# Kernel tuning notes

Measured on AMD Instinct MI355X. Metric: run time of the kernel, lower is better.

The kernel has to match this reference:

```python
import jax, jax.numpy as jnp
import numpy as np

ALPHA = jnp.full((8,), 0.25, dtype=jnp.float32)  # per-class focal alpha
GAMMA = 2.0
TEMP = 0.07
CIRC_TARGET = 1.0
CIRC_WEIGHT = 0.1
MIN_AGREE = 0.6
W_FOCAL, W_CONTRAST, W_CONSENSUS = 1.0, 0.5, 0.3


def setup_inputs() -> dict:
    key = jax.random.key(0)
    k1, k2, k3, k4, k5 = jax.random.split(key, 5)
    return {
        "logits": jax.random.normal(k1, (32, 8, 256, 256), dtype=jnp.float32),
        "target": jax.random.randint(k2, (32, 256, 256), 0, 8, dtype=jnp.int32),
        "features": jax.random.normal(k3, (1024, 512), dtype=jnp.float32),
        "masks": jax.random.uniform(k4, (32, 3, 256, 256), dtype=jnp.float32),
        "method_preds": jax.random.uniform(k5, (3, 32, 256, 256), dtype=jnp.float32),
    }


def focal_loss(logits, target):
    B, C, H, W = logits.shape
    x = logits.transpose(0, 2, 3, 1).reshape(-1, C)  # [BHW, C]
    t = target.reshape(-1)
    logp = jax.nn.log_softmax(x, axis=-1)
    ce = -jnp.take_along_axis(logp, t[:, None], axis=1)[:, 0]
    p = jnp.exp(-ce)
    focal_w = ALPHA[t] * (1.0 - p) ** GAMMA
    return jnp.mean(focal_w * ce)


def contrastive_loss(features):
    Bf = features.shape[0]
    f = features / jnp.linalg.norm(features, axis=1, keepdims=True)
    sim = (f @ f.T) / TEMP  # [Bf, Bf]
    # default labels = arange(Bf//2) tiled twice -> each sample has exactly one
    # positive: its paired view at index (i + Bf//2) % Bf
    pos_idx = (jnp.arange(Bf) + Bf // 2) % Bf
    pos = sim[jnp.arange(Bf), pos_idx]
    diag = jnp.eye(Bf, dtype=bool)
    # logits row i = {positive_i} U negatives_i = all j != i (single positive case)
    masked = jnp.where(diag, -1e30, sim)
    lse = jax.nn.logsumexp(masked, axis=1)
    return jnp.mean(lse - pos)  # CE with target = the (only) positive


def circularity_loss(masks):
    m = masks[:, 0]  # [B, H, W] core channel
    B = m.shape[0]
    area = jnp.sum(m, axis=(1, 2))
    ex = jnp.sum(jnp.abs(m[:, 1:, :] - m[:, :-1, :]), axis=(1, 2))
    ey = jnp.sum(jnp.abs(m[:, :, 1:] - m[:, :, :-1]), axis=(1, 2))
    per = ex + ey
    circ = 4.0 * np.pi * area / jnp.maximum(per, 1e-12) ** 2
    li = jnp.where((area > 0) & (per > 0), (circ - CIRC_TARGET) ** 2, 0.0)
    return CIRC_WEIGHT * jnp.sum(li) / B


def consensus_loss(method_preds):
    K = method_preds.shape[0]
    total, n = 0.0, 0
    for i in range(K):  # K=3 methods -> 3 pairs (fixed, small)
        for j in range(i + 1, K):
            pi, pj = method_preds[i], method_preds[j]
            inter = jnp.sum(pi * pj)
            union = jnp.sum(pi + pj - pi * pj)
            iou = inter / (union + 1e-6)
            total = total + jax.nn.relu(MIN_AGREE - iou)
            n += 1
    return total / n


def reference(logits, target, features, masks, method_preds):
    return (W_FOCAL * focal_loss(logits, target)
            + W_CONTRAST * contrastive_loss(features)
            + circularity_loss(masks)
            + W_CONSENSUS * consensus_loss(method_preds))
```

## Files before the change

kernel.cpp:

```cpp
#include <hip/hip_runtime.h>
#include <math.h>

#define WS_FOCALP 0
#define WS_CONSP  2048
#define WS_AREAP  14336
#define WS_EXP_   14848
#define WS_EYP_   15360
#define WS_POS    15872
#define WS_PART   16896
#define WS_HI_B   393216
#define WS_LO_B   1441792

typedef __attribute__((ext_vector_type(8))) short bf16x8;
typedef __attribute__((ext_vector_type(4))) float f32x4;

__device__ inline float wave_reduce(float v) {
#pragma unroll
  for (int m = 32; m >= 1; m >>= 1) v += __shfl_xor(v, m);
  return v;
}

__device__ inline unsigned short bf16_rne(float x) {
  union { float f; unsigned u; } v; v.f = x;
  unsigned r = v.u + 0x7FFF + ((v.u >> 16) & 1);
  return (unsigned short)(r >> 16);
}
__device__ inline float bf16_f(unsigned short h) {
  union { unsigned u; float f; } v; v.u = ((unsigned)h) << 16; return v.f;
}

__device__ inline float focal_px(float v0, float v1, float v2, float v3,
                                 float v4, float v5, float v6, float v7, int tt) {
  float mx = fmaxf(fmaxf(fmaxf(v0, v1), fmaxf(v2, v3)),
                   fmaxf(fmaxf(v4, v5), fmaxf(v6, v7)));
  float se = expf(v0 - mx) + expf(v1 - mx) + expf(v2 - mx) + expf(v3 - mx) +
             expf(v4 - mx) + expf(v5 - mx) + expf(v6 - mx) + expf(v7 - mx);
  float xt = v0;
  xt = (tt == 1) ? v1 : xt;
  xt = (tt == 2) ? v2 : xt;
  xt = (tt == 3) ? v3 : xt;
  xt = (tt == 4) ? v4 : xt;
  xt = (tt == 5) ? v5 : xt;
  xt = (tt == 6) ? v6 : xt;
  xt = (tt == 7) ? v7 : xt;
  float lp = (xt - mx) - logf(se);
  float p = expf(lp);
  float om = 1.0f - p;
  return 0.25f * om * om * (-lp);
}

__global__ __launch_bounds__(256) void mega_kernel(
    const float* __restrict__ logits, const int* __restrict__ target,
    const float* __restrict__ feat, const float* __restrict__ masks,
    const float* __restrict__ preds, float* __restrict__ ws) {
  __shared__ float red[32];
  const int bid = blockIdx.x;
  const int tid = threadIdx.x;
  const int lane = tid & 63;
  const int wid = tid >> 6;

  if (bid < 2048) {
    int t = bid * 256 + tid;
    int p4 = t * 4;
    int b = p4 >> 16;
    int hw = p4 & 65535;
    const float* lb = logits + (b << 19) + hw;
    float4 x0 = *(const float4*)(lb + (0 << 16));
    float4 x1 = *(const float4*)(lb + (1 << 16));
    float4 x2 = *(const float4*)(lb + (2 << 16));
    float4 x3 = *(const float4*)(lb + (3 << 16));
    float4 x4 = *(const float4*)(lb + (4 << 16));
    float4 x5 = *(const float4*)(lb + (5 << 16));
    float4 x6 = *(const float4*)(lb + (6 << 16));
    float4 x7 = *(const float4*)(lb + (7 << 16));
    int4 tg = *(const int4*)(target + p4);
    float acc = 0.0f;
    acc += focal_px(x0.x, x1.x, x2.x, x3.x, x4.x, x5.x, x6.x, x7.x, tg.x);
    acc += focal_px(x0.y, x1.y, x2.y, x3.y, x4.y, x5.y, x6.y, x7.y, tg.y);
    acc += focal_px(x0.z, x1.z, x2.z, x3.z, x4.z, x5.z, x6.z, x7.z, tg.z);
    acc += focal_px(x0.w, x1.w, x2.w, x3.w, x4.w, x5.w, x6.w, x7.w, tg.w);
    float v = wave_reduce(acc);
    if (lane == 0) red[wid] = v;
    __syncthreads();
    if (tid == 0) ws[WS_FOCALP + bid] = red[0] + red[1] + red[2] + red[3];

  } else if (bid < 2560) {
    int bi = bid - 2048;
    int img = bi >> 4;
    int part = bi & 15;
    const float* mS = masks + img * 3 * 65536;
    const float4* m4 = (const float4*)mS;
    float a = 0.0f, ex = 0.0f, ey = 0.0f;
#pragma unroll
    for (int i = 0; i < 4; i++) {
      int v = tid + 256 * i;
      int rl = v >> 6;
      int c4 = v & 63;
      int row = part * 16 + rl;
      float4 val = m4[row * 64 + c4];
      a += val.x + val.y + val.z + val.w;
      ey += fabsf(val.y - val.x) + fabsf(val.z - val.y) + fabsf(val.w - val.z);
      if (c4 > 0) ey += fabsf(val.x - mS[row * 256 + c4 * 4 - 1]);
      if (row > 0) {
        float4 u = m4[(row - 1) * 64 + c4];
        ex += fabsf(val.x - u.x) + fabsf(val.y - u.y) +
              fabsf(val.z - u.z) + fabsf(val.w - u.w);
      }
    }
    float ra = wave_reduce(a);
    float rx = wave_reduce(ex);
    float ry = wave_reduce(ey);
    if (lane == 0) {
      red[wid + 0] = ra; red[wid + 4] = rx; red[wid + 8] = ry;
    }
    __syncthreads();
    if (tid == 0) {
      ws[WS_AREAP + bi] = red[0] + red[1] + red[2] + red[3];
      ws[WS_EXP_ + bi] = red[4] + red[5] + red[6] + red[7];
      ws[WS_EYP_ + bi] = red[8] + red[9] + red[10] + red[11];
    }

  } else if (bid < 4608) {
    int b = bid - 2560;
    int t = b * 256 + tid;
    const float4* q = (const float4*)preds;
    float4 a0 = q[t];
    float4 a1 = q[t + 524288];
    float4 a2 = q[t + 1048576];
    float s0 = a0.x + a0.y + a0.z + a0.w;
    float s1 = a1.x + a1.y + a1.z + a1.w;
    float s2 = a2.x + a2.y + a2.z + a2.w;
    float p01 = a0.x * a1.x + a0.y * a1.y + a0.z * a1.z + a0.w * a1.w;
    float p02 = a0.x * a2.x + a0.y * a2.y + a0.z * a2.z + a0.w * a2.w;
    float p12 = a1.x * a2.x + a1.y * a2.y + a1.z * a2.z + a1.w * a2.w;
    float r0 = wave_reduce(s0);
    float r1 = wave_reduce(s1);
    float r2 = wave_reduce(s2);
    float r3 = wave_reduce(p01);
    float r4 = wave_reduce(p02);
    float r5 = wave_reduce(p12);
    if (lane == 0) {
      red[wid + 0] = r0; red[wid + 4] = r1; red[wid + 8] = r2;
      red[wid + 12] = r3; red[wid + 16] = r4; red[wid + 20] = r5;
    }
    __syncthreads();
    if (tid == 0) {
#pragma unroll
      for (int k = 0; k < 6; k++)
        ws[WS_CONSP + k * 2048 + b] =
            red[k * 4] + red[k * 4 + 1] + red[k * 4 + 2] + red[k * 4 + 3];
    }

  } else {
    int row = (bid - 4608) * 4 + wid;
    const float4* f4 = (const float4*)feat;
    float4 u = f4[row * 128 + lane];
    float4 w = f4[row * 128 + 64 + lane];
    float s = u.x * u.x + u.y * u.y + u.z * u.z + u.w * u.w +
              w.x * w.x + w.y * w.y + w.z * w.z + w.w * w.w;
    s = wave_reduce(s);
    float scale = 3.7796447300922719f / sqrtf(s);
    float g[8] = {u.x * scale, u.y * scale, u.z * scale, u.w * scale,
                  w.x * scale, w.y * scale, w.z * scale, w.w * scale};
    unsigned short h[8];
    unsigned short l[8];
#pragma unroll
    for (int i = 0; i < 8; i++) {
      h[i] = bf16_rne(g[i]);
      l[i] = bf16_rne(g[i] - bf16_f(h[i]));
    }
    char* hb = (char*)ws + WS_HI_B + row * 1024;
    char* lb = (char*)ws + WS_LO_B + row * 1024;
    *(ushort4*)(hb + lane * 8) = make_ushort4(h[0], h[1], h[2], h[3]);
    *(ushort4*)(hb + 512 + lane * 8) = make_ushort4(h[4], h[5], h[6], h[7]);
    *(ushort4*)(lb + lane * 8) = make_ushort4(l[0], l[1], l[2], l[3]);
    *(ushort4*)(lb + 512 + lane * 8) = make_ushort4(l[4], l[5], l[6], l[7]);
  }
}

__global__ __launch_bounds__(256) void sim_kernel(float* __restrict__ ws) {
  __shared__ __align__(16) char lds[49152];
  const int tid = threadIdx.x;
  const int lane = tid & 63;
  const int wid = tid >> 6;
  const int wr = wid >> 1, wc = wid & 1;
  const int rt = blockIdx.x >> 4, ct = blockIdx.x & 15;
  const int rb = rt * 32, cb = ct * 64;
  const int hi8 = lane >> 4;
  const int l15 = lane & 15;
  const int lr_a = wr * 16 + l15;
  const int rb0 = wc * 32 + l15;
  const int rb1 = rb0 + 16;

  f32x4 acc0 = {0.f, 0.f, 0.f, 0.f};
  f32x4 acc1 = {0.f, 0.f, 0.f, 0.f};

  auto stage = [&](int ch) {
    const char* srcA = (const char*)ws + (ch < 8 ? WS_HI_B : WS_LO_B);
    const char* srcB = (const char*)ws + ((ch >> 2) == 1 ? WS_LO_B : WS_HI_B);
    int koff = (ch & 3) * 256;
    char* dst = lds + (ch & 1) * 24576;
#pragma unroll
    for (int rr = 0; rr < 6; rr++) {
      int idx = rr * 256 + tid;
      const char* g;
      if (rr < 2) {
        int row = idx >> 4, sl = idx & 15;
        g = srcA + (rb + row) * 1024 + koff + ((sl ^ (row & 7)) << 4);
      } else {
        int i2 = idx - 512;
        int row = i2 >> 4, sl = i2 & 15;
        g = srcB + (cb + row) * 1024 + koff + ((sl ^ (row & 7)) << 4);
      }
      __builtin_amdgcn_global_load_lds(
          (const __attribute__((address_space(1))) unsigned int*)g,
          (__attribute__((address_space(3))) unsigned int*)(dst + idx * 16),
          16, 0, 0);
    }
  };

  auto compute = [&](int buf) {
    const char* bp = lds + buf * 24576;
#pragma unroll
    for (int j = 0; j < 4; j++) {
      int sa = (j * 4 + hi8) ^ (lr_a & 7);
      bf16x8 a = *(const bf16x8*)(bp + lr_a * 256 + sa * 16);
      int sb0 = (j * 4 + hi8) ^ (rb0 & 7);
      bf16x8 b0 = *(const bf16x8*)(bp + 8192 + rb0 * 256 + sb0 * 16);
      int sb1 = (j * 4 + hi8) ^ (rb1 & 7);
      bf16x8 b1 = *(const bf16x8*)(bp + 8192 + rb1 * 256 + sb1 * 16);
      acc0 = __builtin_amdgcn_mfma_f32_16x16x32_bf16(a, b0, acc0, 0, 0, 0);
      acc1 = __builtin_amdgcn_mfma_f32_16x16x32_bf16(a, b1, acc1, 0, 0, 0);
    }
  };

  stage(0);
  __syncthreads();
#pragma unroll 1
  for (int ch = 0; ch < 12; ch++) {
    if (ch + 1 < 12) stage(ch + 1);
    compute(ch & 1);
    __syncthreads();
  }

  int c0 = cb + wc * 32 + l15;
  int c1 = c0 + 16;
  float2* part = (float2*)(ws + WS_PART);
#pragma unroll
  for (int q = 0; q < 4; q++) {
    int r = rb + wr * 16 + hi8 * 4 + q;
    float v0 = acc0[q], v1 = acc1[q];
    int pc = (r + 512) & 1023;
    if (c0 == pc) ws[WS_POS + r] = v0;
    if (c1 == pc) ws[WS_POS + r] = v1;
    if (c0 == r) v0 = -1e30f;
    if (c1 == r) v1 = -1e30f;
    float m = fmaxf(v0, v1);
    float s = expf(v0 - m) + expf(v1 - m);
#pragma unroll
    for (int d = 1; d < 16; d <<= 1) {
      float mo = __shfl_xor(m, d), so = __shfl_xor(s, d);
      float nm = fmaxf(m, mo);
      s = s * expf(m - nm) + so * expf(mo - nm);
      m = nm;
    }
    if (l15 == 0) part[r * 32 + ct * 2 + wc] = make_float2(m, s);
  }
}

__device__ inline float block_reduce_1024(float v, float* red) {
  int tid = threadIdx.x;
  v = wave_reduce(v);
  __syncthreads();
  if ((tid & 63) == 0) red[tid >> 6] = v;
  __syncthreads();
  float t = 0.0f;
  if (tid == 0) {
#pragma unroll
    for (int i = 0; i < 16; i++) t += red[i];
  }
  return t;
}

__global__ __launch_bounds__(1024) void final_kernel(float* __restrict__ ws,
                                                     float* __restrict__ out) {
  __shared__ float red[16];
  __shared__ float li_s[32];
  int r = threadIdx.x;

  const float2* part = (const float2*)(ws + WS_PART);
  float M = -1e30f, S = 0.0f;
#pragma unroll
  for (int ctl = 0; ctl < 32; ctl++) {
    float2 p = part[r * 32 + ctl];
    float nm = fmaxf(M, p.x);
    S = S * expf(M - nm) + p.y * expf(p.x - nm);
    M = nm;
  }
  float lse = M + logf(S);
  float contr_sum = block_reduce_1024(lse - ws[WS_POS + r], red);

  float focal_sum =
      block_reduce_1024(ws[WS_FOCALP + r] + ws[WS_FOCALP + r + 1024], red);

  float cons[6];
#pragma unroll
  for (int k = 0; k < 6; k++) {
    const float* p = ws + WS_CONSP + k * 2048;
    cons[k] = block_reduce_1024(p[r] + p[r + 1024], red);
  }

  float li = 0.0f;
  if (r < 512) {
    float a = ws[WS_AREAP + r];
    float ex = ws[WS_EXP_ + r];
    float ey = ws[WS_EYP_ + r];
#pragma unroll
    for (int d = 1; d < 16; d <<= 1) {
      a += __shfl_xor(a, d);
      ex += __shfl_xor(ex, d);
      ey += __shfl_xor(ey, d);
    }
    if ((r & 15) == 0) {
      float per = ex + ey;
      float dd = fmaxf(per, 1e-12f);
      float c = 12.566370614359172f * a / (dd * dd);
      li = (a > 0.0f && per > 0.0f) ? (c - 1.0f) * (c - 1.0f) : 0.0f;
      li_s[r >> 4] = li;
    }
  }
  __syncthreads();

  if (r == 0) {
    float circ = 0.0f;
#pragma unroll
    for (int i = 0; i < 32; i++) circ += li_s[i];
    circ = 0.1f * circ / 32.0f;

    float contr = contr_sum / 1024.0f;
    float focal = focal_sum / 2097152.0f;

    float S0 = cons[0], S1 = cons[1], S2 = cons[2];
    float P01 = cons[3], P02 = cons[4], P12 = cons[5];
    float co = 0.0f;
    co += fmaxf(0.6f - P01 / (S0 + S1 - P01 + 1e-6f), 0.0f);
    co += fmaxf(0.6f - P02 / (S0 + S2 - P02 + 1e-6f), 0.0f);
    co += fmaxf(0.6f - P12 / (S1 + S2 - P12 + 1e-6f), 0.0f);
    co *= (1.0f / 3.0f);

    out[0] = focal + 0.5f * contr + circ + 0.3f * co;
  }
}

extern "C" void kernel_launch(void* const* d_in, const int* in_sizes, int n_in,
                              void* d_out, int out_size, void* d_ws, size_t ws_size,
                              hipStream_t stream) {
  const float* logits = (const float*)d_in[0];
  const int* target = (const int*)d_in[1];
  const float* feat = (const float*)d_in[2];
  const float* masks = (const float*)d_in[3];
  const float* preds = (const float*)d_in[4];
  float* ws = (float*)d_ws;
  float* out = (float*)d_out;

  mega_kernel<<<4864, 256, 0, stream>>>(logits, target, feat, masks, preds, ws);
  sim_kernel<<<512, 256, 0, stream>>>(ws);
  final_kernel<<<1, 1024, 0, stream>>>(ws, out);
}
```

Baseline: 52.05 us.

## Overlap similarity GEMM with streaming reductions and use fast exp/log intrinsics

```diff
diff --git a/kernel.cpp b/kernel.cpp
--- a/kernel.cpp
+++ b/kernel.cpp
@@ -33,8 +33,8 @@
                                  float v4, float v5, float v6, float v7, int tt) {
   float mx = fmaxf(fmaxf(fmaxf(v0, v1), fmaxf(v2, v3)),
                    fmaxf(fmaxf(v4, v5), fmaxf(v6, v7)));
-  float se = expf(v0 - mx) + expf(v1 - mx) + expf(v2 - mx) + expf(v3 - mx) +
-             expf(v4 - mx) + expf(v5 - mx) + expf(v6 - mx) + expf(v7 - mx);
+  float se = __expf(v0 - mx) + __expf(v1 - mx) + __expf(v2 - mx) + __expf(v3 - mx) +
+             __expf(v4 - mx) + __expf(v5 - mx) + __expf(v6 - mx) + __expf(v7 - mx);
   float xt = v0;
   xt = (tt == 1) ? v1 : xt;
   xt = (tt == 2) ? v2 : xt;
@@ -43,24 +43,144 @@
   xt = (tt == 5) ? v5 : xt;
   xt = (tt == 6) ? v6 : xt;
   xt = (tt == 7) ? v7 : xt;
-  float lp = (xt - mx) - logf(se);
-  float p = expf(lp);
+  float lp = (xt - mx) - __logf(se);
+  float p = __expf(lp);
   float om = 1.0f - p;
   return 0.25f * om * om * (-lp);
 }
 
-__global__ __launch_bounds__(256) void mega_kernel(
+__global__ __launch_bounds__(256) void prep_kernel(const float* __restrict__ feat,
+                                                   float* __restrict__ ws) {
+  const int tid = threadIdx.x;
+  const int lane = tid & 63;
+  const int wid = tid >> 6;
+  int row = blockIdx.x * 4 + wid;
+  const float4* f4 = (const float4*)feat;
+  float4 u = f4[row * 128 + lane];
+  float4 w = f4[row * 128 + 64 + lane];
+  float s = u.x * u.x + u.y * u.y + u.z * u.z + u.w * u.w +
+            w.x * w.x + w.y * w.y + w.z * w.z + w.w * w.w;
+  s = wave_reduce(s);
+  float scale = 3.7796447300922719f / sqrtf(s);
+  float g[8] = {u.x * scale, u.y * scale, u.z * scale, u.w * scale,
+                w.x * scale, w.y * scale, w.z * scale, w.w * scale};
+  unsigned short h[8];
+  unsigned short l[8];
+#pragma unroll
+  for (int i = 0; i < 8; i++) {
+    h[i] = bf16_rne(g[i]);
+    l[i] = bf16_rne(g[i] - bf16_f(h[i]));
+  }
+  char* hb = (char*)ws + WS_HI_B + row * 1024;
+  char* lb = (char*)ws + WS_LO_B + row * 1024;
+  *(ushort4*)(hb + lane * 8) = make_ushort4(h[0], h[1], h[2], h[3]);
+  *(ushort4*)(hb + 512 + lane * 8) = make_ushort4(h[4], h[5], h[6], h[7]);
+  *(ushort4*)(lb + lane * 8) = make_ushort4(l[0], l[1], l[2], l[3]);
+  *(ushort4*)(lb + 512 + lane * 8) = make_ushort4(l[4], l[5], l[6], l[7]);
+}
+
+__global__ __launch_bounds__(256) void fused_kernel(
     const float* __restrict__ logits, const int* __restrict__ target,
-    const float* __restrict__ feat, const float* __restrict__ masks,
-    const float* __restrict__ preds, float* __restrict__ ws) {
-  __shared__ float red[32];
+    const float* __restrict__ masks, const float* __restrict__ preds,
+    float* __restrict__ ws) {
+  __shared__ __align__(16) char lds[49152];
   const int bid = blockIdx.x;
   const int tid = threadIdx.x;
   const int lane = tid & 63;
   const int wid = tid >> 6;
 
-  if (bid < 2048) {
-    int t = bid * 256 + tid;
+  if (bid < 512) {
+    const int wr = wid >> 1, wc = wid & 1;
+    const int rt = bid >> 4, ct = bid & 15;
+    const int rb = rt * 32, cb = ct * 64;
+    const int hi8 = lane >> 4;
+    const int l15 = lane & 15;
+    const int lr_a = wr * 16 + l15;
+    const int rb0 = wc * 32 + l15;
+    const int rb1 = rb0 + 16;
+
+    f32x4 acc0 = {0.f, 0.f, 0.f, 0.f};
+    f32x4 acc1 = {0.f, 0.f, 0.f, 0.f};
+
+    auto stage = [&](int ch) {
+      const char* srcA = (const char*)ws + (ch < 8 ? WS_HI_B : WS_LO_B);
+      const char* srcB = (const char*)ws + ((ch >> 2) == 1 ? WS_LO_B : WS_HI_B);
+      int koff = (ch & 3) * 256;
+      char* dst = lds + (ch & 1) * 24576;
+#pragma unroll
+      for (int rr = 0; rr < 6; rr++) {
+        int idx = rr * 256 + tid;
+        const char* g;
+        if (rr < 2) {
+          int row = idx >> 4, sl = idx & 15;
+          g = srcA + (rb + row) * 1024 + koff + ((sl ^ (row & 7)) << 4);
+        } else {
+          int i2 = idx - 512;
+          int row = i2 >> 4, sl = i2 & 15;
+          g = srcB + (cb + row) * 1024 + koff + ((sl ^ (row & 7)) << 4);
+        }
+        __builtin_amdgcn_global_load_lds(
+            (const __attribute__((address_space(1))) unsigned int*)g,
+            (__attribute__((address_space(3))) unsigned int*)(dst + idx * 16),
+            16, 0, 0);
+      }
+    };
+
+    auto compute = [&](int buf) {
+      const char* bp = lds + buf * 24576;
+#pragma unroll
+      for (int j = 0; j < 4; j++) {
+        int sa = (j * 4 + hi8) ^ (lr_a & 7);
+        bf16x8 a = *(const bf16x8*)(bp + lr_a * 256 + sa * 16);
+        int sb0 = (j * 4 + hi8) ^ (rb0 & 7);
+        bf16x8 b0 = *(const bf16x8*)(bp + 8192 + rb0 * 256 + sb0 * 16);
+        int sb1 = (j * 4 + hi8) ^ (rb1 & 7);
+        bf16x8 b1 = *(const bf16x8*)(bp + 8192 + rb1 * 256 + sb1 * 16);
+        acc0 = __builtin_amdgcn_mfma_f32_16x16x32_bf16(a, b0, acc0, 0, 0, 0);
+        acc1 = __builtin_amdgcn_mfma_f32_16x16x32_bf16(a, b1, acc1, 0, 0, 0);
+      }
+    };
+
+    stage(0);
+    __syncthreads();
+#pragma unroll 1
+    for (int ch = 0; ch < 12; ch++) {
+      if (ch + 1 < 12) stage(ch + 1);
+      compute(ch & 1);
+      __syncthreads();
+    }
+
+    int c0 = cb + wc * 32 + l15;
+    int c1 = c0 + 16;
+    float2* part = (float2*)(ws + WS_PART);
+#pragma unroll
+    for (int q = 0; q < 4; q++) {
+      int r = rb + wr * 16 + hi8 * 4 + q;
+      float v0 = acc0[q], v1 = acc1[q];
+      int pc = (r + 512) & 1023;
+      if (c0 == pc) ws[WS_POS + r] = v0;
+      if (c1 == pc) ws[WS_POS + r] = v1;
+      if (c0 == r) v0 = -1e30f;
+      if (c1 == r) v1 = -1e30f;
+      float m = fmaxf(v0, v1);
+      float s = __expf(v0 - m) + __expf(v1 - m);
+#pragma unroll
+      for (int d = 1; d < 16; d <<= 1) {
+        float mo = __shfl_xor(m, d), so = __shfl_xor(s, d);
+        float nm = fmaxf(m, mo);
+        s = s * __expf(m - nm) + so * __expf(mo - nm);
+        m = nm;
+      }
+      if (l15 == 0) part[r * 32 + ct * 2 + wc] = make_float2(m, s);
+    }
+    return;
+  }
+
+  float* red = (float*)lds;
+  const int bid2 = bid - 512;
+
+  if (bid2 < 2048) {
+    int t = bid2 * 256 + tid;
     int p4 = t * 4;
     int b = p4 >> 16;
     int hw = p4 & 65535;
@@ -82,10 +202,10 @@
     float v = wave_reduce(acc);
     if (lane == 0) red[wid] = v;
     __syncthreads();
-    if (tid == 0) ws[WS_FOCALP + bid] = red[0] + red[1] + red[2] + red[3];
-
-  } else if (bid < 2560) {
-    int bi = bid - 2048;
+    if (tid == 0) ws[WS_FOCALP + bid2] = red[0] + red[1] + red[2] + red[3];
+
+  } else if (bid2 < 2560) {
+    int bi = bid2 - 2048;
     int img = bi >> 4;
     int part = bi & 15;
     const float* mS = masks + img * 3 * 65536;
@@ -120,8 +240,8 @@
       ws[WS_EYP_ + bi] = red[8] + red[9] + red[10] + red[11];
     }
 
-  } else if (bid < 4608) {
-    int b = bid - 2560;
+  } else {
+    int b = bid2 - 2560;
     int t = b * 256 + tid;
     const float4* q = (const float4*)preds;
     float4 a0 = q[t];
@@ -150,121 +270,6 @@
         ws[WS_CONSP + k * 2048 + b] =
             red[k * 4] + red[k * 4 + 1] + red[k * 4 + 2] + red[k * 4 + 3];
     }
-
-  } else {
-    int row = (bid - 4608) * 4 + wid;
-    const float4* f4 = (const float4*)feat;
-    float4 u = f4[row * 128 + lane];
-    float4 w = f4[row * 128 + 64 + lane];
-    float s = u.x * u.x + u.y * u.y + u.z * u.z + u.w * u.w +
-              w.x * w.x + w.y * w.y + w.z * w.z + w.w * w.w;
-    s = wave_reduce(s);
-    float scale = 3.7796447300922719f / sqrtf(s);
-    float g[8] = {u.x * scale, u.y * scale, u.z * scale, u.w * scale,
-                  w.x * scale, w.y * scale, w.z * scale, w.w * scale};
-    unsigned short h[8];
-    unsigned short l[8];
-#pragma unroll
-    for (int i = 0; i < 8; i++) {
-      h[i] = bf16_rne(g[i]);
-      l[i] = bf16_rne(g[i] - bf16_f(h[i]));
-    }
-    char* hb = (char*)ws + WS_HI_B + row * 1024;
-    char* lb = (char*)ws + WS_LO_B + row * 1024;
-    *(ushort4*)(hb + lane * 8) = make_ushort4(h[0], h[1], h[2], h[3]);
-    *(ushort4*)(hb + 512 + lane * 8) = make_ushort4(h[4], h[5], h[6], h[7]);
-    *(ushort4*)(lb + lane * 8) = make_ushort4(l[0], l[1], l[2], l[3]);
-    *(ushort4*)(lb + 512 + lane * 8) = make_ushort4(l[4], l[5], l[6], l[7]);
-  }
-}
-
-__global__ __launch_bounds__(256) void sim_kernel(float* __restrict__ ws) {
-  __shared__ __align__(16) char lds[49152];
-  const int tid = threadIdx.x;
-  const int lane = tid & 63;
-  const int wid = tid >> 6;
-  const int wr = wid >> 1, wc = wid & 1;
-  const int rt = blockIdx.x >> 4, ct = blockIdx.x & 15;
-  const int rb = rt * 32, cb = ct * 64;
-  const int hi8 = lane >> 4;
-  const int l15 = lane & 15;
-  const int lr_a = wr * 16 + l15;
-  const int rb0 = wc * 32 + l15;
-  const int rb1 = rb0 + 16;
-
-  f32x4 acc0 = {0.f, 0.f, 0.f, 0.f};
-  f32x4 acc1 = {0.f, 0.f, 0.f, 0.f};
-
-  auto stage = [&](int ch) {
-    const char* srcA = (const char*)ws + (ch < 8 ? WS_HI_B : WS_LO_B);
-    const char* srcB = (const char*)ws + ((ch >> 2) == 1 ? WS_LO_B : WS_HI_B);
-    int koff = (ch & 3) * 256;
-    char* dst = lds + (ch & 1) * 24576;
-#pragma unroll
-    for (int rr = 0; rr < 6; rr++) {
-      int idx = rr * 256 + tid;
-      const char* g;
-      if (rr < 2) {
-        int row = idx >> 4, sl = idx & 15;
-        g = srcA + (rb + row) * 1024 + koff + ((sl ^ (row & 7)) << 4);
-      } else {
-        int i2 = idx - 512;
-        int row = i2 >> 4, sl = i2 & 15;
-        g = srcB + (cb + row) * 1024 + koff + ((sl ^ (row & 7)) << 4);
-      }
-      __builtin_amdgcn_global_load_lds(
-          (const __attribute__((address_space(1))) unsigned int*)g,
-          (__attribute__((address_space(3))) unsigned int*)(dst + idx * 16),
-          16, 0, 0);
-    }
-  };
-
-  auto compute = [&](int buf) {
-    const char* bp = lds + buf * 24576;
-#pragma unroll
-    for (int j = 0; j < 4; j++) {
-      int sa = (j * 4 + hi8) ^ (lr_a & 7);
-      bf16x8 a = *(const bf16x8*)(bp + lr_a * 256 + sa * 16);
-      int sb0 = (j * 4 + hi8) ^ (rb0 & 7);
-      bf16x8 b0 = *(const bf16x8*)(bp + 8192 + rb0 * 256 + sb0 * 16);
-      int sb1 = (j * 4 + hi8) ^ (rb1 & 7);
-      bf16x8 b1 = *(const bf16x8*)(bp + 8192 + rb1 * 256 + sb1 * 16);
-      acc0 = __builtin_amdgcn_mfma_f32_16x16x32_bf16(a, b0, acc0, 0, 0, 0);
-      acc1 = __builtin_amdgcn_mfma_f32_16x16x32_bf16(a, b1, acc1, 0, 0, 0);
-    }
-  };
-
-  stage(0);
-  __syncthreads();
-#pragma unroll 1
-  for (int ch = 0; ch < 12; ch++) {
-    if (ch + 1 < 12) stage(ch + 1);
-    compute(ch & 1);
-    __syncthreads();
-  }
-
-  int c0 = cb + wc * 32 + l15;
-  int c1 = c0 + 16;
-  float2* part = (float2*)(ws + WS_PART);
-#pragma unroll
-  for (int q = 0; q < 4; q++) {
-    int r = rb + wr * 16 + hi8 * 4 + q;
-    float v0 = acc0[q], v1 = acc1[q];
-    int pc = (r + 512) & 1023;
-    if (c0 == pc) ws[WS_POS + r] = v0;
-    if (c1 == pc) ws[WS_POS + r] = v1;
-    if (c0 == r) v0 = -1e30f;
-    if (c1 == r) v1 = -1e30f;
-    float m = fmaxf(v0, v1);
-    float s = expf(v0 - m) + expf(v1 - m);
-#pragma unroll
-    for (int d = 1; d < 16; d <<= 1) {
-      float mo = __shfl_xor(m, d), so = __shfl_xor(s, d);
-      float nm = fmaxf(m, mo);
-      s = s * expf(m - nm) + so * expf(mo - nm);
-      m = nm;
-    }
-    if (l15 == 0) part[r * 32 + ct * 2 + wc] = make_float2(m, s);
   }
 }
 
@@ -294,10 +299,10 @@
   for (int ctl = 0; ctl < 32; ctl++) {
     float2 p = part[r * 32 + ctl];
     float nm = fmaxf(M, p.x);
-    S = S * expf(M - nm) + p.y * expf(p.x - nm);
+    S = S * __expf(M - nm) + p.y * __expf(p.x - nm);
     M = nm;
   }
-  float lse = M + logf(S);
+  float lse = M + __logf(S);
   float contr_sum = block_reduce_1024(lse - ws[WS_POS + r], red);
 
   float focal_sum =
@@ -363,7 +368,7 @@
   float* ws = (float*)d_ws;
   float* out = (float*)d_out;
 
-  mega_kernel<<<4864, 256, 0, stream>>>(logits, target, feat, masks, preds, ws);
-  sim_kernel<<<512, 256, 0, stream>>>(ws);
+  prep_kernel<<<256, 256, 0, stream>>>(feat, ws);
+  fused_kernel<<<5120, 256, 0, stream>>>(logits, target, masks, preds, ws);
   final_kernel<<<1, 1024, 0, stream>>>(ws, out);
 }
```

New measurement: 50.18 us. 1.04x faster.
